# Optimization experiments

Measured on AMD Instinct MI355X. Metric: run time of the kernel, lower is better.

## Reference

```python
import jax, jax.numpy as jnp
import numpy as np

N_NODES = 100000

def _sage_conv(h, src, dst, Wl, bl, Wr):
    # PyG SAGEConv (mean aggr): out = lin_l(mean_{j in N(i)} h_j) + lin_r(h_i)
    msg = h[src]                                            # [E, H] gather
    agg = jax.ops.segment_sum(msg, dst, num_segments=N_NODES)   # [N, H] scatter-add
    cnt = jax.ops.segment_sum(jnp.ones((src.shape[0],), h.dtype), dst, num_segments=N_NODES)
    mean = agg / jnp.maximum(cnt, 1.0)[:, None]
    return mean @ Wl + bl + h @ Wr

def setup_inputs() -> dict:
    key = jax.random.key(0)
    ks = jax.random.split(key, 12)
    IN, H, C, E = 256, 128, 40, 1600000
    s = 0.05
    return {
        "x": jax.random.normal(ks[0], (N_NODES, IN), jnp.float32),
        "edge_index": jax.random.randint(ks[1], (2, E), 0, N_NODES, jnp.int32),
        "W_pre": jax.random.normal(ks[2], (IN, H), jnp.float32) * s,
        "b_pre": jnp.zeros((H,), jnp.float32),
        "Wl0": jax.random.normal(ks[3], (H, H), jnp.float32) * s,
        "bl0": jnp.zeros((H,), jnp.float32),
        "Wr0": jax.random.normal(ks[4], (H, H), jnp.float32) * s,
        "Wl1": jax.random.normal(ks[5], (H, H), jnp.float32) * s,
        "bl1": jnp.zeros((H,), jnp.float32),
        "Wr1": jax.random.normal(ks[6], (H, H), jnp.float32) * s,
        "W_post": jax.random.normal(ks[7], (H, C), jnp.float32) * s,
        "b_post": jnp.zeros((C,), jnp.float32),
    }

def reference(x, edge_index, W_pre, b_pre, Wl0, bl0, Wr0, Wl1, bl1, Wr1, W_post, b_post):
    src, dst = edge_index[0], edge_index[1]
    h = x @ W_pre + b_pre                       # pre Linear
    # two SAGEConv layers + relu (dropout is identity in eval mode)
    h = jax.nn.relu(_sage_conv(h, src, dst, Wl0, bl0, Wr0))
    h = jax.nn.relu(_sage_conv(h, src, dst, Wl1, bl1, Wr1))
    logits = h @ W_post + b_post                # post Linear
    return jax.nn.log_softmax(logits, axis=1)
```

## Files before the change

kernel.cpp:

```cpp
#include <hip/hip_runtime.h>
#include <hip/hip_bf16.h>
#include <math.h>

#define N_NODES 100000
#define IN_F 256
#define HID 128
#define NCLS 40

#define NB 782
#define BN 128
#define NC 448
#define CSZ2 3584

typedef __attribute__((ext_vector_type(8))) short short8;
typedef __attribute__((ext_vector_type(4))) float f32x4;

__device__ __forceinline__ short f2bf(float f){
  union { float f; unsigned u; } x; x.f = f;
  unsigned r = (x.u + 0x7fffu + ((x.u >> 16) & 1u)) >> 16;
  return (short)r;
}
__device__ __forceinline__ float bf2f(unsigned short u){
  union { unsigned u; float f; } x; x.u = ((unsigned)u) << 16;
  return x.f;
}
__device__ __forceinline__ unsigned char f2i8(float v){
  float q = fmaf(v, 16.f, 128.5f);
  q = fminf(fmaxf(q, 0.f), 255.f);
  return (unsigned char)q;
}

__global__ __launch_bounds__(256) void k_wprep(
    const float* __restrict__ Wpre, const float* __restrict__ Wl0,
    const float* __restrict__ Wr0,  const float* __restrict__ Wl1,
    const float* __restrict__ Wr1,  const float* __restrict__ Wpost,
    unsigned short* __restrict__ img)
{
  const int g = blockIdx.x*256 + threadIdx.x;
  if(g >= 13056) return;
  const int base = g*8;
  unsigned short v[8];
  if(base < 98304){
    const int which = base >> 15;
    const int idx = base & 32767;
    const int l = (idx >> 3) & 63, kb = (idx >> 9) & 7, ct = idx >> 12;
    const int col = ct*16 + (l & 15);
    const float* Wsrc; int kbase;
    if(which == 0){ Wsrc = Wpre; kbase = kb*32 + (l>>4)*8; }
    else{
      Wsrc = (which==1) ? ((kb<4) ? Wl0 : Wr0) : ((kb<4) ? Wl1 : Wr1);
      kbase = (kb&3)*32 + (l>>4)*8;
    }
    #pragma unroll
    for(int j = 0; j < 8; j++) v[j] = (unsigned short)f2bf(Wsrc[(size_t)(kbase+j)*HID + col]);
  } else {
    const int idx = base - 98304;
    const int l = (idx >> 3) & 63, kb = (idx >> 9) & 3, ct = idx >> 11;
    const int col = ct*16 + (l & 15);
    const int kbase = kb*32 + (l>>4)*8;
    #pragma unroll
    for(int j = 0; j < 8; j++)
      v[j] = (col < NCLS) ? (unsigned short)f2bf(Wpost[(size_t)(kbase+j)*NCLS + col]) : 0;
  }
  *reinterpret_cast<short8*>(img + base) = *reinterpret_cast<const short8*>(v);
}

__global__ __launch_bounds__(256) void k_hist(const int* __restrict__ dst, int E,
                                              int* __restrict__ cnt){
  __shared__ int hist[NB];
  const int c = blockIdx.x;
  for(int i = threadIdx.x; i < NB; i += 256) hist[i] = 0;
  __syncthreads();
  const int s0 = c*CSZ2, s1 = min(s0 + CSZ2, E);
  for(int i = s0 + threadIdx.x; i < s1; i += 256)
    atomicAdd(&hist[(unsigned)__builtin_nontemporal_load(dst + i) >> 7], 1);
  __syncthreads();
  for(int i = threadIdx.x; i < NB; i += 256) cnt[c*NB + i] = hist[i];
}

__global__ __launch_bounds__(256) void k_bscanA(const int* __restrict__ cnt,
                                                int* __restrict__ wbase,
                                                int* __restrict__ btot){
  __shared__ int s[256];
  const int b = blockIdx.x;
  const int t = threadIdx.x;
  int v0 = 0, v1 = 0;
  if(2*t < NC)     v0 = cnt[(2*t)*NB + b];
  if(2*t + 1 < NC) v1 = cnt[(2*t+1)*NB + b];
  s[t] = v0 + v1; __syncthreads();
  for(int d = 1; d < 256; d <<= 1){
    int add = (t >= d) ? s[t-d] : 0;
    __syncthreads();
    s[t] += add;
    __syncthreads();
  }
  const int ex = (t > 0) ? s[t-1] : 0;
  if(2*t < NC)     wbase[(2*t)*NB + b] = ex;
  if(2*t + 1 < NC) wbase[(2*t+1)*NB + b] = ex + v0;
  if(t == 255) btot[b] = s[255];
}

__global__ __launch_bounds__(1024) void k_bscanB(const int* __restrict__ btot,
                                                 int* __restrict__ bstart, int E){
  __shared__ int s[1024];
  const int t = threadIdx.x;
  int v = (t < NB) ? btot[t] : 0;
  s[t] = v; __syncthreads();
  for(int d = 1; d < 1024; d <<= 1){
    int add = (t >= d) ? s[t-d] : 0;
    __syncthreads();
    s[t] += add;
    __syncthreads();
  }
  if(t < NB) bstart[t] = s[t] - v;
  if(t == 0) bstart[NB] = E;
}

__global__ __launch_bounds__(256) void k_place(const int* __restrict__ src,
                                               const int* __restrict__ dst, int E,
                                               const int* __restrict__ wbase,
                                               const int* __restrict__ bstart,
                                               int* __restrict__ pk){
  const int g = blockIdx.x;
  const int c = (g & 7)*(NC/8) + (g >> 3);
  __shared__ int cur[NB];
  for(int i = threadIdx.x; i < NB; i += 256)
    cur[i] = wbase[c*NB + i] + bstart[i];
  __syncthreads();
  const int s0 = c*CSZ2, s1 = min(s0 + CSZ2, E);
  for(int i = s0 + threadIdx.x; i < s1; i += 256){
    const int d  = __builtin_nontemporal_load(dst + i);
    const int sv = __builtin_nontemporal_load(src + i);
    const int pos = atomicAdd(&cur[(unsigned)d >> 7], 1);
    pk[pos] = ((d & 127) << 17) | sv;
  }
}

__global__ __launch_bounds__(512) void k_sortb(const int* __restrict__ pk,
                                               const int* __restrict__ bstart,
                                               int* __restrict__ esrc2,
                                               int* __restrict__ nodeoff, int E){
  __shared__ int hist[BN];
  __shared__ int nofs[BN];
  __shared__ int curs[BN];
  const int b = blockIdx.x;
  const int t = threadIdx.x;
  const int bs = bstart[b];
  const int ne = bstart[b+1] - bs;
  for(int i = t; i < BN; i += 512) hist[i] = 0;
  __syncthreads();
  for(int i = t; i < ne; i += 512)
    atomicAdd(&hist[(unsigned)pk[bs + i] >> 17], 1);
  __syncthreads();
  if(t < BN) nofs[t] = hist[t];
  __syncthreads();
  for(int d = 1; d < BN; d <<= 1){
    int add = 0;
    if(t < BN && t >= d) add = nofs[t-d];
    __syncthreads();
    if(t < BN) nofs[t] += add;
    __syncthreads();
  }
  if(t < BN){
    curs[t] = nofs[t] - hist[t];
    const int node = b*BN + t;
    if(node < N_NODES) nodeoff[node] = bs + nofs[t] - hist[t];
    if(node == N_NODES - 1 || (b == NB-1 && t == BN-1)) nodeoff[N_NODES] = E;
  }
  __syncthreads();
  for(int i = t; i < ne; i += 512){
    const int e = pk[bs + i];
    const int pos = atomicAdd(&curs[(unsigned)e >> 17], 1);
    esrc2[bs + pos] = e & 0x1ffff;
  }
}

__global__ __launch_bounds__(256) void k_agg3(
    const unsigned short* __restrict__ h, const int* __restrict__ nodeoff,
    const int* __restrict__ esrc2, unsigned short* __restrict__ mean)
{
  const int lane = threadIdx.x & 63;
  const int wid = blockIdx.x*4 + (threadIdx.x >> 6);
  const int wstride = gridDim.x*4;
  const unsigned* hp = (const unsigned*)h;
  for(int node = wid; node < N_NODES; node += wstride){
    const int beg = nodeoff[node];
    const int deg = nodeoff[node+1] - beg;
    float a0 = 0.f, a1 = 0.f;
    for(int base = 0; base < deg; base += 64){
      const int rem = deg - base;
      const int cnt = rem < 64 ? rem : 64;
      const int myi = (lane < cnt) ? esrc2[beg + base + lane] : 0;
      int e = 0;
      for(; e + 8 <= cnt; e += 8){
        unsigned v[8];
        #pragma unroll
        for(int u = 0; u < 8; u++){
          const int s = __builtin_amdgcn_readlane(myi, e + u);
          v[u] = hp[(size_t)s*64 + lane];
        }
        #pragma unroll
        for(int u = 0; u < 8; u++){
          a0 += bf2f((unsigned short)(v[u] & 0xffffu));
          a1 += bf2f((unsigned short)(v[u] >> 16));
        }
      }
      for(; e < cnt; e++){
        const int s = __builtin_amdgcn_readlane(myi, e);
        const unsigned vv = hp[(size_t)s*64 + lane];
        a0 += bf2f((unsigned short)(vv & 0xffffu));
        a1 += bf2f((unsigned short)(vv >> 16));
      }
    }
    const float inv = (deg > 0) ? (1.0f/(float)deg) : 0.f;
    a0 *= inv; a1 *= inv;
    const unsigned o = ((unsigned)(unsigned short)f2bf(a1) << 16) | (unsigned)(unsigned short)f2bf(a0);
    ((unsigned*)mean)[(size_t)node*64 + lane] = o;
  }
}

__global__ __launch_bounds__(256) void k_agg8(
    const unsigned char* __restrict__ h8, const int* __restrict__ nodeoff,
    const int* __restrict__ esrc2, unsigned short* __restrict__ mean)
{
  const int lane = threadIdx.x & 63;
  const int wid = blockIdx.x*4 + (threadIdx.x >> 6);
  const int wstride = gridDim.x*4;
  const unsigned short* hp = (const unsigned short*)h8;
  for(int node = wid; node < N_NODES; node += wstride){
    const int beg = nodeoff[node];
    const int deg = nodeoff[node+1] - beg;
    float a0 = 0.f, a1 = 0.f;
    for(int base = 0; base < deg; base += 64){
      const int rem = deg - base;
      const int cnt = rem < 64 ? rem : 64;
      const int myi = (lane < cnt) ? esrc2[beg + base + lane] : 0;
      int e = 0;
      for(; e + 16 <= cnt; e += 16){
        unsigned short v[16];
        #pragma unroll
        for(int u = 0; u < 16; u++)
          v[u] = hp[(size_t)__builtin_amdgcn_readlane(myi, e + u)*64 + lane];
        #pragma unroll
        for(int u = 0; u < 16; u++){
          a0 += (float)(v[u] & 0xffu);
          a1 += (float)(v[u] >> 8);
        }
      }
      for(; e + 8 <= cnt; e += 8){
        unsigned short v[8];
        #pragma unroll
        for(int u = 0; u < 8; u++)
          v[u] = hp[(size_t)__builtin_amdgcn_readlane(myi, e + u)*64 + lane];
        #pragma unroll
        for(int u = 0; u < 8; u++){
          a0 += (float)(v[u] & 0xffu);
          a1 += (float)(v[u] >> 8);
        }
      }
      for(; e < cnt; e++){
        const unsigned short vv = hp[(size_t)__builtin_amdgcn_readlane(myi, e)*64 + lane];
        a0 += (float)(vv & 0xffu);
        a1 += (float)(vv >> 8);
      }
    }
    float m0 = 0.f, m1 = 0.f;
    if(deg > 0){
      const float inv = 1.0f/(float)deg;
      m0 = (a0*inv - 128.f)*0.0625f;
      m1 = (a1*inv - 128.f)*0.0625f;
    }
    const unsigned o = ((unsigned)(unsigned short)f2bf(m1) << 16) | (unsigned)(unsigned short)f2bf(m0);
    ((unsigned*)mean)[(size_t)node*64 + lane] = o;
  }
}

__global__ __launch_bounds__(256) void k_gemm_pre(
    const float* __restrict__ x, const unsigned short* __restrict__ wimg,
    const float* __restrict__ b, unsigned short* __restrict__ out,
    unsigned char* __restrict__ h8)
{
  const int t = threadIdx.x;
  const int wave = t >> 6, lane = t & 63;
  const int r_in = lane & 15, kg = lane >> 4;
  const int tile = blockIdx.x*4 + wave;
  if(tile >= N_NODES/16) return;
  const int row0 = tile*16;
  const float* xp = x + (size_t)(row0 + r_in)*IN_F + kg*8;

  float4 xa0[4], xb0[4], xa1[4], xb1[4];
  #pragma unroll
  for(int kb = 0; kb < 4; kb++){
    xa0[kb] = *reinterpret_cast<const float4*>(xp + kb*32);
    xb0[kb] = *reinterpret_cast<const float4*>(xp + kb*32 + 4);
  }
  #pragma unroll
  for(int kb = 0; kb < 4; kb++){
    xa1[kb] = *reinterpret_cast<const float4*>(xp + (kb+4)*32);
    xb1[kb] = *reinterpret_cast<const float4*>(xp + (kb+4)*32 + 4);
  }
  f32x4 acc[8];
  #pragma unroll
  for(int ct = 0; ct < 8; ct++) acc[ct] = (f32x4){0.f,0.f,0.f,0.f};
  #pragma unroll
  for(int kb = 0; kb < 4; kb++){
    short8 a;
    a[0]=f2bf(xa0[kb].x); a[1]=f2bf(xa0[kb].y); a[2]=f2bf(xa0[kb].z); a[3]=f2bf(xa0[kb].w);
    a[4]=f2bf(xb0[kb].x); a[5]=f2bf(xb0[kb].y); a[6]=f2bf(xb0[kb].z); a[7]=f2bf(xb0[kb].w);
    #pragma unroll
    for(int ct = 0; ct < 8; ct++){
      short8 bb = *reinterpret_cast<const short8*>(wimg + ((ct*8+kb)*64+lane)*8);
      acc[ct] = __builtin_amdgcn_mfma_f32_16x16x32_bf16(a, bb, acc[ct], 0, 0, 0);
    }
  }
  #pragma unroll
  for(int kb = 4; kb < 8; kb++){
    short8 a;
    a[0]=f2bf(xa1[kb-4].x); a[1]=f2bf(xa1[kb-4].y); a[2]=f2bf(xa1[kb-4].z); a[3]=f2bf(xa1[kb-4].w);
    a[4]=f2bf(xb1[kb-4].x); a[5]=f2bf(xb1[kb-4].y); a[6]=f2bf(xb1[kb-4].z); a[7]=f2bf(xb1[kb-4].w);
    #pragma unroll
    for(int ct = 0; ct < 8; ct++){
      short8 bb = *reinterpret_cast<const short8*>(wimg + ((ct*8+kb)*64+lane)*8);
      acc[ct] = __builtin_amdgcn_mfma_f32_16x16x32_bf16(a, bb, acc[ct], 0, 0, 0);
    }
  }
  #pragma unroll
  for(int ct = 0; ct < 8; ct++){
    const int col = ct*16 + r_in;
    const float bias = b[col];
    #pragma unroll
    for(int i = 0; i < 4; i++){
      const int row = row0 + kg*4 + i;
      const float v = acc[ct][i] + bias;
      out[(size_t)row*HID + col] = (unsigned short)f2bf(v);
      if(h8) h8[(size_t)row*HID + col] = f2i8(v);
    }
  }
}

__global__ __launch_bounds__(256) void k_gemm_sage(
    const unsigned short* __restrict__ mean, const unsigned short* __restrict__ h,
    const unsigned short* __restrict__ wimg, const float* __restrict__ bl,
    unsigned short* __restrict__ out, unsigned char* __restrict__ h8out)
{
  __shared__ short wlds[8*8*64*8];
  const int t = threadIdx.x;
  {
    short8* dstp = reinterpret_cast<short8*>(wlds);
    const short8* srcp = reinterpret_cast<const short8*>(wimg);
    #pragma unroll
    for(int i = 0; i < 16; i++) dstp[t + i*256] = srcp[t + i*256];
  }
  __syncthreads();
  const int wave = t >> 6, lane = t & 63;
  const int r_in = lane & 15, kg = lane >> 4;
  const int NT = N_NODES/16, stride = gridDim.x*4;

  auto loadx = [&](int tile, short8 (&am)[4], short8 (&ah)[4]){
    const size_t base = (size_t)(tile*16 + r_in)*HID + kg*8;
    #pragma unroll
    for(int kb = 0; kb < 4; kb++){
      am[kb] = *reinterpret_cast<const short8*>(mean + base + kb*32);
      ah[kb] = *reinterpret_cast<const short8*>(h    + base + kb*32);
    }
  };
  auto compute = [&](int tile, const short8 (&am)[4], const short8 (&ah)[4]){
    f32x4 acc[8];
    #pragma unroll
    for(int ct = 0; ct < 8; ct++) acc[ct] = (f32x4){0.f,0.f,0.f,0.f};
    #pragma unroll
    for(int kb = 0; kb < 8; kb++){
      short8 a = (kb < 4) ? am[kb & 3] : ah[kb & 3];
      #pragma unroll
      for(int ct = 0; ct < 8; ct++){
        short8 bb = *reinterpret_cast<const short8*>(&wlds[((ct*8+kb)*64+lane)*8]);
        acc[ct] = __builtin_amdgcn_mfma_f32_16x16x32_bf16(a, bb, acc[ct], 0, 0, 0);
      }
    }
    const int row0 = tile*16;
    #pragma unroll
    for(int ct = 0; ct < 8; ct++){
      const int col = ct*16 + r_in;
      const float bias = bl[col];
      #pragma unroll
      for(int i = 0; i < 4; i++){
        const int row = row0 + kg*4 + i;
        float v = fmaxf(acc[ct][i] + bias, 0.f);
        out[(size_t)row*HID + col] = (unsigned short)f2bf(v);
        if(h8out) h8out[(size_t)row*HID + col] = f2i8(v);
      }
    }
  };

  int tile = blockIdx.x*4 + wave;
  if(tile >= NT) return;
  short8 amA[4], ahA[4], amB[4], ahB[4];
  loadx(tile, amA, ahA);
  for(;;){
    int nt = tile + stride;
    bool more = nt < NT;
    if(more) loadx(nt, amB, ahB);
    compute(tile, amA, ahA);
    if(!more) break;
    tile = nt;
    nt = tile + stride;
    more = nt < NT;
    if(more) loadx(nt, amA, ahA);
    compute(tile, amB, ahB);
    if(!more) break;
    tile = nt;
  }
}

__global__ __launch_bounds__(256) void k_post(
    const unsigned short* __restrict__ h, const unsigned short* __restrict__ wimg,
    const float* __restrict__ b, float* __restrict__ out)
{
  __shared__ short wlds[3*4*64*8];
  __shared__ float bias_s[48];
  const int t = threadIdx.x;
  {
    short8* dstp = reinterpret_cast<short8*>(wlds);
    const short8* srcp = reinterpret_cast<const short8*>(wimg);
    for(int i = t; i < 768; i += 256) dstp[i] = srcp[i];
  }
  if(t < 48) bias_s[t] = (t < NCLS) ? b[t] : -1e30f;
  __syncthreads();
  const int wave = t >> 6, lane = t & 63;
  const int r_in = lane & 15, kg = lane >> 4;
  for(int tile = blockIdx.x*4 + wave; tile < N_NODES/16; tile += gridDim.x*4){
    const int row0 = tile*16;
    f32x4 acc[3];
    #pragma unroll
    for(int ct = 0; ct < 3; ct++) acc[ct] = (f32x4){0.f,0.f,0.f,0.f};
    #pragma unroll
    for(int kb = 0; kb < 4; kb++){
      short8 a = *reinterpret_cast<const short8*>(h + (size_t)(row0 + r_in)*HID + kb*32 + kg*8);
      #pragma unroll
      for(int ct = 0; ct < 3; ct++){
        short8 bb = *reinterpret_cast<const short8*>(&wlds[((ct*4+kb)*64+lane)*8]);
        acc[ct] = __builtin_amdgcn_mfma_f32_16x16x32_bf16(a, bb, acc[ct], 0, 0, 0);
      }
    }
    #pragma unroll
    for(int i = 0; i < 4; i++){
      float v0 = acc[0][i] + bias_s[r_in];
      float v1 = acc[1][i] + bias_s[16 + r_in];
      float v2 = acc[2][i] + bias_s[32 + r_in];
      float m = fmaxf(fmaxf(v0, v1), v2);
      #pragma unroll
      for(int o = 8; o > 0; o >>= 1) m = fmaxf(m, __shfl_xor(m, o));
      float s = expf(v0 - m) + expf(v1 - m) + expf(v2 - m);
      #pragma unroll
      for(int o = 8; o > 0; o >>= 1) s += __shfl_xor(s, o);
      const float ls = m + logf(s);
      const int row = row0 + kg*4 + i;
      float* op = out + (size_t)row*NCLS;
      op[r_in] = v0 - ls;
      op[16 + r_in] = v1 - ls;
      if(r_in < 8) op[32 + r_in] = v2 - ls;
    }
  }
}

extern "C" void kernel_launch(void* const* d_in, const int* in_sizes, int n_in,
                              void* d_out, int out_size, void* d_ws, size_t ws_size,
                              hipStream_t stream)
{
  const float* x      = (const float*)d_in[0];
  const int*   ei     = (const int*)  d_in[1];
  const float* W_pre  = (const float*)d_in[2];
  const float* b_pre  = (const float*)d_in[3];
  const float* Wl0    = (const float*)d_in[4];
  const float* bl0    = (const float*)d_in[5];
  const float* Wr0    = (const float*)d_in[6];
  const float* Wl1    = (const float*)d_in[7];
  const float* bl1    = (const float*)d_in[8];
  const float* Wr1    = (const float*)d_in[9];
  const float* W_post = (const float*)d_in[10];
  const float* b_post = (const float*)d_in[11];
  float* out = (float*)d_out;

  const int E = in_sizes[1] / 2;
  const int* src = ei;
  const int* dst = ei + E;

  char* ws = (char*)d_ws;
  size_t off = 0;
  auto alloc = [&](size_t bytes)->void*{
    void* p = ws + off;
    off += (bytes + 255) & ~(size_t)255;
    return p;
  };
  unsigned short* hA = (unsigned short*)alloc((size_t)N_NODES*HID*2);
  unsigned short* hB = (unsigned short*)alloc((size_t)N_NODES*HID*2);
  unsigned short* hM = (unsigned short*)alloc((size_t)N_NODES*HID*2);
  int* pk      = (int*)alloc((size_t)E*4);
  int* esrc2   = (int*)alloc((size_t)E*4);
  int* cnt     = (int*)alloc((size_t)NC*NB*4);
  int* wbase   = (int*)alloc((size_t)NC*NB*4);
  int* btot    = (int*)alloc((size_t)NB*4);
  int* bstart  = (int*)alloc((size_t)(NB+1)*4);
  int* nodeoff = (int*)alloc((size_t)(N_NODES+1)*4);
  unsigned short* wimg = (unsigned short*)alloc(104448*2);
  unsigned char* h8A = (unsigned char*)alloc((size_t)N_NODES*HID);
  unsigned char* h8B = (unsigned char*)alloc((size_t)N_NODES*HID);
  const bool use8 = (off <= ws_size);

  k_wprep<<<51, 256, 0, stream>>>(W_pre, Wl0, Wr0, Wl1, Wr1, W_post, wimg);

  k_hist<<<NC, 256, 0, stream>>>(dst, E, cnt);
  k_bscanA<<<NB, 256, 0, stream>>>(cnt, wbase, btot);
  k_bscanB<<<1, 1024, 0, stream>>>(btot, bstart, E);
  k_place<<<NC, 256, 0, stream>>>(src, dst, E, wbase, bstart, pk);
  k_sortb<<<NB, 512, 0, stream>>>(pk, bstart, esrc2, nodeoff, E);

  k_gemm_pre<<<1563, 256, 0, stream>>>(x, wimg, b_pre, hA, use8 ? h8A : nullptr);

  if(use8){
    k_agg8<<<4096, 256, 0, stream>>>(h8A, nodeoff, esrc2, hM);
    k_gemm_sage<<<512, 256, 0, stream>>>(hM, hA, wimg + 32768, bl0, hB, h8B);
    k_agg8<<<4096, 256, 0, stream>>>(h8B, nodeoff, esrc2, hM);
    k_gemm_sage<<<512, 256, 0, stream>>>(hM, hB, wimg + 65536, bl1, hA, nullptr);
  } else {
    k_agg3<<<4096, 256, 0, stream>>>(hA, nodeoff, esrc2, hM);
    k_gemm_sage<<<512, 256, 0, stream>>>(hM, hA, wimg + 32768, bl0, hB, nullptr);
    k_agg3<<<4096, 256, 0, stream>>>(hB, nodeoff, esrc2, hM);
    k_gemm_sage<<<512, 256, 0, stream>>>(hM, hB, wimg + 65536, bl1, hA, nullptr);
  }

  k_post<<<1563, 256, 0, stream>>>(hA, wimg + 98304, b_post, out);
}
```

Measured before the change: 250.1 us.

## Make pre-GEMM persistent with LDS-staged weights and double-buffered x prefetch

The pre-linear GEMM kernel now copies its bf16 weight image into LDS once per block and reads B fragments from shared memory instead of global memory. It becomes a grid-stride persistent kernel launched with 512 blocks, with each wave walking several 16-row tiles. The fp32 input for the next tile is loaded into a second register buffer while the current tile is computed. The aim is to overlap the large x read with MFMA work and amortise weight loading, at the cost of higher register pressure (two 16-float4 buffers) and 64KB of LDS per block, which may reduce occupancy.

```diff
diff --git a/kernel.cpp b/kernel.cpp
--- a/kernel.cpp
+++ b/kernel.cpp
@@ -280,61 +280,74 @@
     const float* __restrict__ b, unsigned short* __restrict__ out,
     unsigned char* __restrict__ h8)
 {
+  __shared__ short wlds[8*8*64*8];
   const int t = threadIdx.x;
+  {
+    short8* dstp = reinterpret_cast<short8*>(wlds);
+    const short8* srcp = reinterpret_cast<const short8*>(wimg);
+    #pragma unroll
+    for(int i = 0; i < 16; i++) dstp[t + i*256] = srcp[t + i*256];
+  }
+  __syncthreads();
   const int wave = t >> 6, lane = t & 63;
   const int r_in = lane & 15, kg = lane >> 4;
-  const int tile = blockIdx.x*4 + wave;
-  if(tile >= N_NODES/16) return;
-  const int row0 = tile*16;
-  const float* xp = x + (size_t)(row0 + r_in)*IN_F + kg*8;
-
-  float4 xa0[4], xb0[4], xa1[4], xb1[4];
-  #pragma unroll
-  for(int kb = 0; kb < 4; kb++){
-    xa0[kb] = *reinterpret_cast<const float4*>(xp + kb*32);
-    xb0[kb] = *reinterpret_cast<const float4*>(xp + kb*32 + 4);
-  }
-  #pragma unroll
-  for(int kb = 0; kb < 4; kb++){
-    xa1[kb] = *reinterpret_cast<const float4*>(xp + (kb+4)*32);
-    xb1[kb] = *reinterpret_cast<const float4*>(xp + (kb+4)*32 + 4);
-  }
-  f32x4 acc[8];
-  #pragma unroll
-  for(int ct = 0; ct < 8; ct++) acc[ct] = (f32x4){0.f,0.f,0.f,0.f};
-  #pragma unroll
-  for(int kb = 0; kb < 4; kb++){
-    short8 a;
-    a[0]=f2bf(xa0[kb].x); a[1]=f2bf(xa0[kb].y); a[2]=f2bf(xa0[kb].z); a[3]=f2bf(xa0[kb].w);
-    a[4]=f2bf(xb0[kb].x); a[5]=f2bf(xb0[kb].y); a[6]=f2bf(xb0[kb].z); a[7]=f2bf(xb0[kb].w);
+  const int NT = N_NODES/16, stride = gridDim.x*4;
+
+  auto loadx = [&](int tile, float4 (&xa)[8], float4 (&xb)[8]){
+    const float* xp = x + (size_t)(tile*16 + r_in)*IN_F + kg*8;
+    #pragma unroll
+    for(int kb = 0; kb < 8; kb++){
+      xa[kb] = *reinterpret_cast<const float4*>(xp + kb*32);
+      xb[kb] = *reinterpret_cast<const float4*>(xp + kb*32 + 4);
+    }
+  };
+  auto compute = [&](int tile, const float4 (&xa)[8], const float4 (&xb)[8]){
+    f32x4 acc[8];
+    #pragma unroll
+    for(int ct = 0; ct < 8; ct++) acc[ct] = (f32x4){0.f,0.f,0.f,0.f};
+    #pragma unroll
+    for(int kb = 0; kb < 8; kb++){
+      short8 a;
+      a[0]=f2bf(xa[kb].x); a[1]=f2bf(xa[kb].y); a[2]=f2bf(xa[kb].z); a[3]=f2bf(xa[kb].w);
+      a[4]=f2bf(xb[kb].x); a[5]=f2bf(xb[kb].y); a[6]=f2bf(xb[kb].z); a[7]=f2bf(xb[kb].w);
+      #pragma unroll
+      for(int ct = 0; ct < 8; ct++){
+        short8 bb = *reinterpret_cast<const short8*>(&wlds[((ct*8+kb)*64+lane)*8]);
+        acc[ct] = __builtin_amdgcn_mfma_f32_16x16x32_bf16(a, bb, acc[ct], 0, 0, 0);
+      }
+    }
+    const int row0 = tile*16;
     #pragma unroll
     for(int ct = 0; ct < 8; ct++){
-      short8 bb = *reinterpret_cast<const short8*>(wimg + ((ct*8+kb)*64+lane)*8);
-      acc[ct] = __builtin_amdgcn_mfma_f32_16x16x32_bf16(a, bb, acc[ct], 0, 0, 0);
-    }
-  }
-  #pragma unroll
-  for(int kb = 4; kb < 8; kb++){
-    short8 a;
-    a[0]=f2bf(xa1[kb-4].x); a[1]=f2bf(xa1[kb-4].y); a[2]=f2bf(xa1[kb-4].z); a[3]=f2bf(xa1[kb-4].w);
-    a[4]=f2bf(xb1[kb-4].x); a[5]=f2bf(xb1[kb-4].y); a[6]=f2bf(xb1[kb-4].z); a[7]=f2bf(xb1[kb-4].w);
-    #pragma unroll
-    for(int ct = 0; ct < 8; ct++){
-      short8 bb = *reinterpret_cast<const short8*>(wimg + ((ct*8+kb)*64+lane)*8);
-      acc[ct] = __builtin_amdgcn_mfma_f32_16x16x32_bf16(a, bb, acc[ct], 0, 0, 0);
-    }
-  }
-  #pragma unroll
-  for(int ct = 0; ct < 8; ct++){
-    const int col = ct*16 + r_in;
-    const float bias = b[col];
-    #pragma unroll
-    for(int i = 0; i < 4; i++){
-      const int row = row0 + kg*4 + i;
-      const float v = acc[ct][i] + bias;
-      out[(size_t)row*HID + col] = (unsigned short)f2bf(v);
-      if(h8) h8[(size_t)row*HID + col] = f2i8(v);
-    }
+      const int col = ct*16 + r_in;
+      const float bias = b[col];
+      #pragma unroll
+      for(int i = 0; i < 4; i++){
+        const int row = row0 + kg*4 + i;
+        const float v = acc[ct][i] + bias;
+        out[(size_t)row*HID + col] = (unsigned short)f2bf(v);
+        if(h8) h8[(size_t)row*HID + col] = f2i8(v);
+      }
+    }
+  };
+
+  int tile = blockIdx.x*4 + wave;
+  if(tile >= NT) return;
+  float4 xaA[8], xbA[8], xaB[8], xbB[8];
+  loadx(tile, xaA, xbA);
+  for(;;){
+    int nt = tile + stride;
+    bool more = nt < NT;
+    if(more) loadx(nt, xaB, xbB);
+    compute(tile, xaA, xbA);
+    if(!more) break;
+    tile = nt;
+    nt = tile + stride;
+    more = nt < NT;
+    if(more) loadx(nt, xaA, xbA);
+    compute(tile, xaB, xbB);
+    if(!more) break;
+    tile = nt;
   }
 }
 
@@ -515,7 +528,7 @@
   k_place<<<NC, 256, 0, stream>>>(src, dst, E, wbase, bstart, pk);
   k_sortb<<<NB, 512, 0, stream>>>(pk, bstart, esrc2, nodeoff, E);
 
-  k_gemm_pre<<<1563, 256, 0, stream>>>(x, wimg, b_pre, hA, use8 ? h8A : nullptr);
+  k_gemm_pre<<<512, 256, 0, stream>>>(x, wimg, b_pre, hA, use8 ? h8A : nullptr);
 
   if(use8){
     k_agg8<<<4096, 256, 0, stream>>>(h8A, nodeoff, esrc2, hM);
```

Measured after the change: 243.5 us. 2.6% less time.
